# Performance work log

Measured on AMD Instinct MI355X. Metric: run time of the kernel, lower is better.

The kernel has to match this reference:

```python
import jax, jax.numpy as jnp
import numpy as np

BATCH = 2
SEQ = 2048
DIM = 2048
HEADS = 16
DIM_HEAD = 64
DIM_INNER = HEADS * DIM_HEAD  # 1024
SOFTCAP = 50.0
EPS = 1e-12


def setup_inputs() -> dict:
    key = jax.random.key(0)
    k1, k2, k3, k4 = jax.random.split(key, 4)
    x = jax.random.normal(k1, (BATCH, SEQ, DIM), dtype=jnp.float32)
    # RMSNorm gamma param (initialized near zero in the torch module)
    gamma = jax.random.normal(k2, (DIM,), dtype=jnp.float32) * 0.02
    # Linear weights stored already-transposed: x @ W
    w_qkv = jax.random.normal(k3, (DIM, 3 * DIM_INNER), dtype=jnp.float32) * (DIM ** -0.5)
    w_out = jax.random.normal(k4, (DIM_INNER, DIM), dtype=jnp.float32) * (DIM_INNER ** -0.5)
    # (type, offset, length) triples per batch; bidirectional attention inside each span
    modalities = jnp.array(
        [[[0, 256, 256], [0, 1024, 512]],
         [[0, 128, 256], [0, 1536, 384]]], dtype=jnp.int32)
    return dict(x=x, gamma=gamma, w_qkv=w_qkv, w_out=w_out, modalities=modalities)


def _transfusion_attn_mask(seq_len, modalities):
    # causal | (q in span AND kv in span)  -> Bool[b, i, j]
    seq = jnp.arange(seq_len)
    causal = seq[:, None] >= seq[None, :]                      # [i, j]
    offsets = modalities[..., 1]                                # [b, m]
    ends = offsets + modalities[..., 2]                         # [b, m]
    q_in = seq[None, None, :] >= offsets[..., None]             # [b, m, i]
    kv_in = seq[None, None, :] < ends[..., None]                # [b, m, j]
    is_modality = jnp.any(q_in[..., :, None] & kv_in[..., None, :], axis=1)  # [b, i, j]
    return causal[None] | is_modality


def _rmsnorm(x, gamma):
    n = jnp.sqrt(jnp.sum(x * x, axis=-1, keepdims=True))
    x = x / jnp.maximum(n, EPS)
    return x * (DIM ** 0.5) * (gamma + 1.0)


def reference(x, gamma, w_qkv, w_out, modalities):
    xn = _rmsnorm(x, gamma)
    qkv = xn @ w_qkv                                            # [b, n, 3*h*d]
    qkv = qkv.reshape(BATCH, SEQ, 3, HEADS, DIM_HEAD)
    qkv = jnp.transpose(qkv, (2, 0, 3, 1, 4))                   # [3, b, h, n, d]
    q, k, v = qkv[0], qkv[1], qkv[2]
    q = q * (DIM_HEAD ** -0.5)
    sim = jnp.einsum('bhid,bhjd->bhij', q, k)
    sim = jnp.tanh(sim / SOFTCAP) * SOFTCAP                     # softclamp
    mask = _transfusion_attn_mask(SEQ, modalities)              # [b, i, j]
    neg = -jnp.finfo(sim.dtype).max
    sim = jnp.where(mask[:, None, :, :], sim, neg)
    attn = jax.nn.softmax(sim, axis=-1)
    out = jnp.einsum('bhij,bhjd->bhid', attn, v)
    out = jnp.transpose(out, (0, 2, 1, 3)).reshape(BATCH, SEQ, DIM_INNER)
    return out @ w_out
```

## Files before the change

kernel.cpp:

```cpp
#include <hip/hip_runtime.h>
#include <hip/hip_bf16.h>

typedef unsigned short u16;
typedef unsigned int u32;
typedef __attribute__((ext_vector_type(8))) short short8;
typedef __attribute__((ext_vector_type(4))) float f32x4;
typedef __attribute__((ext_vector_type(4))) u16 u16x4;

#define DEV __device__ __forceinline__

DEV u16 f2bf(float f) {
    union { float f; u32 u; } v; v.f = f;
    u32 r = v.u;
    u32 lsb = (r >> 16) & 1u;
    r += 0x7fffu + lsb;
    return (u16)(r >> 16);
}

DEV void gload_lds16(const u16* g, u16* l) {
    __builtin_amdgcn_global_load_lds(
        (const __attribute__((address_space(1))) u32*)(const void*)g,
        (__attribute__((address_space(3))) u32*)(void*)l,
        16, 0, 0);
}

__global__ void prep(const float* __restrict__ x, const float* __restrict__ gamma,
                     const float* __restrict__ w_qkv, const float* __restrict__ w_out,
                     u16* __restrict__ xn, u16* __restrict__ wqkvT, u16* __restrict__ woutT) {
    __shared__ float tile[32][33];
    __shared__ float red[4];
    int id = blockIdx.x;
    int t = threadIdx.x;
    if (id < 8192) {
        const float* in; u16* out; int R, C, bx, by;
        if (id < 6144) { in = w_qkv; out = wqkvT; R = 2048; C = 3072; bx = id % 96; by = id / 96; }
        else { id -= 6144; in = w_out; out = woutT; R = 1024; C = 2048; bx = id % 64; by = id / 64; }
        int tx = t & 31, ty = t >> 5;
        int c0 = bx * 32, r0 = by * 32;
#pragma unroll
        for (int i = 0; i < 4; i++)
            tile[ty * 4 + i][tx] = in[(size_t)(r0 + ty * 4 + i) * C + c0 + tx];
        __syncthreads();
#pragma unroll
        for (int i = 0; i < 4; i++)
            out[(size_t)(c0 + ty * 4 + i) * R + r0 + tx] = f2bf(tile[tx][ty * 4 + i]);
    } else {
        int row = id - 8192;
        const float4* xr = (const float4*)(x + (size_t)row * 2048);
        float4 a = xr[t];
        float4 b = xr[256 + t];
        float ss = a.x * a.x + a.y * a.y + a.z * a.z + a.w * a.w +
                   b.x * b.x + b.y * b.y + b.z * b.z + b.w * b.w;
#pragma unroll
        for (int off = 32; off; off >>= 1) ss += __shfl_xor(ss, off);
        if ((t & 63) == 0) red[t >> 6] = ss;
        __syncthreads();
        float tot = red[0] + red[1] + red[2] + red[3];
        float n = sqrtf(tot);
        float inv = 45.254833995939045f / fmaxf(n, 1e-12f);
        const float4* gr = (const float4*)gamma;
        float4 g0 = gr[t], g1 = gr[256 + t];
        u16x4 o0 = { f2bf(a.x * inv * (g0.x + 1.f)), f2bf(a.y * inv * (g0.y + 1.f)),
                     f2bf(a.z * inv * (g0.z + 1.f)), f2bf(a.w * inv * (g0.w + 1.f)) };
        u16x4 o1 = { f2bf(b.x * inv * (g1.x + 1.f)), f2bf(b.y * inv * (g1.y + 1.f)),
                     f2bf(b.z * inv * (g1.z + 1.f)), f2bf(b.w * inv * (g1.w + 1.f)) };
        u16x4* xo = (u16x4*)(xn + (size_t)row * 2048);
        xo[t] = o0;
        xo[256 + t] = o1;
    }
}

template <int EPI, int BN, int CR, int CC>
__global__ __launch_bounds__(512, 6) void gemmw(
    const u16* __restrict__ A, const u16* __restrict__ BT,
    int M, int N, int K,
    float* __restrict__ Cout,
    u16* __restrict__ qb, u16* __restrict__ kb, u16* __restrict__ vT) {
    constexpr int NF = BN / 64;
    constexpr bool BX = (BN * 4) > 512;
    __shared__ __align__(16) u16 As[3][4096];
    __shared__ __align__(16) u16 Bs[3][BN * 32];
    int t = threadIdx.x, lane = t & 63, wid = t >> 6;
    int g = lane >> 4, r = lane & 15;
    int wm = wid >> 2, wn = wid & 3;
    int csw = (r >> 1) & 3;

    int id = blockIdx.x;
    int xcd = id & 7, slot = id >> 3;
    int by = (xcd >> 1) * CR + slot / CC;
    int bx = (xcd & 1) * CC + slot % CC;
    int brow = by * 128, bcol = bx * BN;

    int gk = (t & 3) ^ ((t >> 3) & 3);
    const u16* Ag = A + (size_t)(brow + (t >> 2)) * K + gk * 8;
    const u16* Bg = BT + (size_t)(bcol + (t >> 2)) * K + gk * 8;
    const u16* Bg2 = BT + (size_t)(bcol + 128 + (t >> 2)) * K + gk * 8;
    int dst = (t & ~63) * 8;

    f32x4 acc[4][NF] = {};
    short8 areg[4], breg[NF];
    int NT = K >> 5;

#define STG(kt_, b3_) { \
        gload_lds16(Ag + (kt_) * 32, &As[b3_][dst]); \
        gload_lds16(Bg + (kt_) * 32, &Bs[b3_][dst]); \
        if constexpr (BX) { if (t < 256) gload_lds16(Bg2 + (kt_) * 32, &Bs[b3_][4096 + dst]); } }
#define SCHEDB() __builtin_amdgcn_sched_barrier(0)
#define BAR() __builtin_amdgcn_s_barrier()

    STG(0, 0);
    if (NT > 1) STG(1, 1);
    asm volatile("s_waitcnt vmcnt(0)" ::: "memory");
    SCHEDB();
    BAR();

    int c0 = 0;
    for (int kt = 0; kt < NT; ++kt) {
        int c2 = c0 + 2; if (c2 >= 3) c2 -= 3;
        bool s1 = kt + 1 < NT, s2 = kt + 2 < NT;
        if (s2) STG(kt + 2, c2);
        const u16* Ac = As[c0];
        const u16* Bc = Bs[c0];
#pragma unroll
        for (int mf = 0; mf < 4; mf++)
            areg[mf] = *(const short8*)&Ac[(wm * 64 + mf * 16 + r) * 32 + (g ^ csw) * 8];
#pragma unroll
        for (int nf = 0; nf < NF; nf++)
            breg[nf] = *(const short8*)&Bc[(wn * (BN / 4) + nf * 16 + r) * 32 + (g ^ csw) * 8];
        asm volatile("s_waitcnt lgkmcnt(0)" ::: "memory");
        SCHEDB();
        __builtin_amdgcn_s_setprio(1);
#pragma unroll
        for (int mf = 0; mf < 4; mf++)
#pragma unroll
            for (int nf = 0; nf < NF; nf++)
                acc[mf][nf] = __builtin_amdgcn_mfma_f32_16x16x32_bf16(areg[mf], breg[nf], acc[mf][nf], 0, 0, 0);
        __builtin_amdgcn_s_setprio(0);
        if (s2) {
            if (BX && wid < 4) { asm volatile("s_waitcnt vmcnt(3)" ::: "memory"); }
            else               { asm volatile("s_waitcnt vmcnt(2)" ::: "memory"); }
        } else if (s1) {
            asm volatile("s_waitcnt vmcnt(0)" ::: "memory");
        }
        SCHEDB();
        BAR();
        c0 = (c0 + 1 == 3) ? 0 : c0 + 1;
    }
#undef STG
#undef SCHEDB
#undef BAR

    if (EPI == 0) {
#pragma unroll
        for (int mf = 0; mf < 4; mf++)
#pragma unroll
            for (int nf = 0; nf < NF; nf++) {
                int cb = bcol + wn * (BN / 4) + nf * 16 + r;
                int which = cb >> 10;
                int hd = cb & 1023;
                int hh = hd >> 6, d = hd & 63;
#pragma unroll
                for (int j = 0; j < 4; j++) {
                    int rr = brow + wm * 64 + mf * 16 + 4 * g + j;
                    int b = rr >> 11, nn = rr & 2047;
                    float v = acc[mf][nf][j];
                    size_t bh = (size_t)(b * 16 + hh);
                    if (which == 0)      qb[(bh * 2048 + nn) * 64 + d] = f2bf(v * 0.125f);
                    else if (which == 1) kb[(bh * 2048 + nn) * 64 + d] = f2bf(v);
                    else                 vT[(bh * 64 + d) * 2048 + nn] = f2bf(v);
                }
            }
    } else {
#pragma unroll
        for (int mf = 0; mf < 4; mf++)
#pragma unroll
            for (int nf = 0; nf < NF; nf++) {
                int cb = bcol + wn * (BN / 4) + nf * 16 + r;
#pragma unroll
                for (int j = 0; j < 4; j++) {
                    int rr = brow + wm * 64 + mf * 16 + 4 * g + j;
                    Cout[(size_t)rr * N + cb] = acc[mf][nf][j];
                }
            }
    }
}

__global__ __launch_bounds__(256, 3) void flash_attn(
    const u16* __restrict__ q, const u16* __restrict__ kk, const u16* __restrict__ vT,
    const int* __restrict__ mods, u16* __restrict__ attn_out) {
    __shared__ __align__(16) u16 Ks[2][4096];
    __shared__ __align__(16) u16 Vs[2][4096];
    __shared__ __align__(16) u16 Plds[4][2][16][72];
    int t = threadIdx.x, lane = t & 63, wave = t >> 6;
    int g = lane >> 4, r = lane & 15;
    int h = blockIdx.x, b = blockIdx.y;
    int qs = (15 - blockIdx.z) * 128;
    int bh = b * 16 + h;
    int qbase = qs + wave * 32;

    int off0 = mods[b * 6 + 1], end0 = off0 + mods[b * 6 + 2];
    int off1 = mods[b * 6 + 4], end1 = off1 + mods[b * 6 + 5];

    const u16* Qp = q + ((size_t)bh * 2048 + qbase) * 64;
    short8 qf0[2], qf1[2];
#pragma unroll
    for (int s = 0; s < 2; s++) {
        qf0[s] = *(const short8*)(Qp + (size_t)(s * 16 + r) * 64 + 8 * g);
        qf1[s] = *(const short8*)(Qp + (size_t)(s * 16 + r) * 64 + 32 + 8 * g);
    }

    int rowlim[2];
#pragma unroll
    for (int s = 0; s < 2; s++) {
        int iq = qbase + s * 16 + r;
        int lim0 = (iq >= off0) ? end0 : 0;
        int lim1 = (iq >= off1) ? end1 : 0;
        rowlim[s] = max(iq + 1, max(lim0, lim1));
    }

    int jlb = qs + 128;
    if (qs + 127 >= off0) jlb = max(jlb, end0);
    if (qs + 127 >= off1) jlb = max(jlb, end1);

    const u16* Kp = kk + (size_t)bh * 2048 * 64;
    const u16* Vp = vT + (size_t)bh * 64 * 2048;

    f32x4 ot[2][4] = {};
    float psA[2] = {}, psB[2] = {};
    int sw = r & 7;

    auto stage64 = [&](const u16* gbase, int gstride, u16* lds) {
#pragma unroll
        for (int i = 0; i < 2; i++) {
            int c = i * 256 + t;
            int row = c >> 3;
            int gsl = (c & 7) ^ (row & 7);
            gload_lds16(gbase + (size_t)row * gstride + 8 * gsl,
                        lds + (size_t)(c & ~63) * 8);
        }
    };

    stage64(Kp, 64, Ks[0]);
    stage64(Vp, 2048, Vs[0]);
    int buf = 0;

    for (int jb = 0; jb < jlb; jb += 64) {
        if (jb + 64 < jlb) {
            stage64(Kp + (size_t)(jb + 64) * 64, 64, Ks[buf ^ 1]);
            stage64(Vp + (jb + 64), 2048, Vs[buf ^ 1]);
            asm volatile("s_waitcnt vmcnt(4)" ::: "memory");
        } else {
            asm volatile("s_waitcnt vmcnt(0)" ::: "memory");
        }
        __builtin_amdgcn_s_barrier();
        const u16* Kt = Ks[buf];
        const u16* Vt = Vs[buf];

        f32x4 st[2][4];
#pragma unroll
        for (int tt = 0; tt < 4; tt++) {
            int row = 16 * tt + r;
            short8 kf0 = *(const short8*)&Kt[(size_t)(row * 8 + (g ^ sw)) * 8];
            short8 kf1 = *(const short8*)&Kt[(size_t)(row * 8 + ((4 + g) ^ sw)) * 8];
#pragma unroll
            for (int s = 0; s < 2; s++) {
                f32x4 z = {};
                z = __builtin_amdgcn_mfma_f32_16x16x32_bf16(kf0, qf0[s], z, 0, 0, 0);
                z = __builtin_amdgcn_mfma_f32_16x16x32_bf16(kf1, qf1[s], z, 0, 0, 0);
                st[s][tt] = z;
            }
        }
#pragma unroll
        for (int s = 0; s < 2; s++) {
            u16* Pws = &Plds[wave][s][0][0];
#pragma unroll
            for (int tt = 0; tt < 4; tt++) {
                int kvb = jb + 16 * tt + 4 * g;
                float p0, p1, p2, p3;
#pragma unroll
                for (int j = 0; j < 4; j++) {
                    float x = st[s][tt][j];
                    float x2 = x * x;
                    float inner = __builtin_fmaf(x2, 2.1333333e-8f, -1.3333333e-4f);
                    float poly = __builtin_fmaf(x2, inner, 1.0f);
                    float pv = __expf(x * poly);
                    pv = (kvb + j < rowlim[s]) ? pv : 0.f;
                    if (j == 0) p0 = pv; else if (j == 1) p1 = pv;
                    else if (j == 2) p2 = pv; else p3 = pv;
                }
                psA[s] += p0 + p1;
                psB[s] += p2 + p3;
                u32 pk0, pk1;
                asm("v_cvt_pk_bf16_f32 %0, %1, %2" : "=v"(pk0) : "v"(p0), "v"(p1));
                asm("v_cvt_pk_bf16_f32 %0, %1, %2" : "=v"(pk1) : "v"(p2), "v"(p3));
                *(u32*)&Pws[r * 72 + 16 * tt + 4 * g] = pk0;
                *(u32*)&Pws[r * 72 + 16 * tt + 4 * g + 2] = pk1;
            }
        }
        short8 pf0[2], pf1[2];
#pragma unroll
        for (int s = 0; s < 2; s++) {
            pf0[s] = *(const short8*)&Plds[wave][s][r][8 * g];
            pf1[s] = *(const short8*)&Plds[wave][s][r][32 + 8 * g];
        }
#pragma unroll
        for (int dt = 0; dt < 4; dt++) {
            int row = 16 * dt + r;
            short8 vf0 = *(const short8*)&Vt[(size_t)(row * 8 + (g ^ sw)) * 8];
            short8 vf1 = *(const short8*)&Vt[(size_t)(row * 8 + ((4 + g) ^ sw)) * 8];
#pragma unroll
            for (int s = 0; s < 2; s++) {
                ot[s][dt] = __builtin_amdgcn_mfma_f32_16x16x32_bf16(vf0, pf0[s], ot[s][dt], 0, 0, 0);
                ot[s][dt] = __builtin_amdgcn_mfma_f32_16x16x32_bf16(vf1, pf1[s], ot[s][dt], 0, 0, 0);
            }
        }
        asm volatile("s_waitcnt lgkmcnt(0)" ::: "memory");
        __builtin_amdgcn_s_barrier();
        buf ^= 1;
    }

#pragma unroll
    for (int s = 0; s < 2; s++) {
        float lrow = psA[s] + psB[s];
        lrow += __shfl_xor(lrow, 16);
        lrow += __shfl_xor(lrow, 32);
        float inv = 1.f / lrow;
        u16* Op = attn_out + ((size_t)(b * 2048 + qbase + s * 16 + r)) * 1024 + h * 64;
#pragma unroll
        for (int dt = 0; dt < 4; dt++) {
            u16x4 o = { f2bf(ot[s][dt][0] * inv), f2bf(ot[s][dt][1] * inv),
                        f2bf(ot[s][dt][2] * inv), f2bf(ot[s][dt][3] * inv) };
            *(u16x4*)(Op + dt * 16 + 4 * g) = o;
        }
    }
}

extern "C" void kernel_launch(void* const* d_in, const int* in_sizes, int n_in,
                              void* d_out, int out_size, void* d_ws, size_t ws_size,
                              hipStream_t stream) {
    const float* x = (const float*)d_in[0];
    const float* gamma = (const float*)d_in[1];
    const float* w_qkv = (const float*)d_in[2];
    const float* w_out = (const float*)d_in[3];
    const int* mods = (const int*)d_in[4];
    float* out = (float*)d_out;

    u16* ws = (u16*)d_ws;
    u16* xn    = ws;
    u16* wqkvT = ws + 8388608;
    u16* woutT = ws + 14680064;
    u16* qb    = ws + 16777216;
    u16* kb    = ws + 20971520;
    u16* vT    = ws + 25165824;
    u16* ao    = ws + 29360128;

    prep<<<dim3(12288), dim3(256), 0, stream>>>(x, gamma, w_qkv, w_out, xn, wqkvT, woutT);
    gemmw<0, 128, 8, 12><<<dim3(768), dim3(512), 0, stream>>>(xn, wqkvT, 4096, 3072, 2048,
                                                              nullptr, qb, kb, vT);
    flash_attn<<<dim3(16, 2, 16), dim3(256), 0, stream>>>(qb, kb, vT, mods, ao);
    gemmw<1, 128, 8, 8><<<dim3(512), dim3(512), 0, stream>>>(ao, woutT, 4096, 2048, 1024,
                                                             out, nullptr, nullptr, nullptr);
}
```

Before: 173.1 us.

## Load GEMM A operand directly from global into registers, bypassing LDS

The A tile is no longer staged through shared memory. Each wave now loads its own A fragments from global memory straight into registers, double-buffered two k-steps ahead, while B stays in the triple-buffered LDS pipeline. This removes the LDS writes and reads for A and shrinks shared memory use, which may allow more blocks per CU. In exchange it adds uncoalesced 16-byte global loads and extra register pressure. The BN>128 branch for loading B is dropped, and the loop is unrolled by two, which assumes NT is even.

```diff
diff --git a/kernel.cpp b/kernel.cpp
--- a/kernel.cpp
+++ b/kernel.cpp
@@ -77,8 +77,6 @@
     float* __restrict__ Cout,
     u16* __restrict__ qb, u16* __restrict__ kb, u16* __restrict__ vT) {
     constexpr int NF = BN / 64;
-    constexpr bool BX = (BN * 4) > 512;
-    __shared__ __align__(16) u16 As[3][4096];
     __shared__ __align__(16) u16 Bs[3][BN * 32];
     int t = threadIdx.x, lane = t & 63, wid = t >> 6;
     int g = lane >> 4, r = lane & 15;
@@ -92,63 +90,61 @@
     int brow = by * 128, bcol = bx * BN;
 
     int gk = (t & 3) ^ ((t >> 3) & 3);
-    const u16* Ag = A + (size_t)(brow + (t >> 2)) * K + gk * 8;
     const u16* Bg = BT + (size_t)(bcol + (t >> 2)) * K + gk * 8;
-    const u16* Bg2 = BT + (size_t)(bcol + 128 + (t >> 2)) * K + gk * 8;
     int dst = (t & ~63) * 8;
 
+    const u16* Arow0 = A + (size_t)(brow + wm * 64 + r) * K + g * 8;
+    const size_t r16K = (size_t)16 * K;
+
     f32x4 acc[4][NF] = {};
-    short8 areg[4], breg[NF];
+    short8 arA[4], arB[4], breg[NF];
     int NT = K >> 5;
 
-#define STG(kt_, b3_) { \
-        gload_lds16(Ag + (kt_) * 32, &As[b3_][dst]); \
-        gload_lds16(Bg + (kt_) * 32, &Bs[b3_][dst]); \
-        if constexpr (BX) { if (t < 256) gload_lds16(Bg2 + (kt_) * 32, &Bs[b3_][4096 + dst]); } }
+#define STGB(kt_, b3_) gload_lds16(Bg + (kt_) * 32, &Bs[b3_][dst]);
+#define LDA(dst_, kt_) { \
+    _Pragma("unroll") for (int mf = 0; mf < 4; mf++) \
+        dst_[mf] = *(const short8*)(Arow0 + (size_t)mf * r16K + (kt_) * 32); }
+#define MFMAS(ar_) { \
+    __builtin_amdgcn_s_setprio(1); \
+    _Pragma("unroll") for (int mf = 0; mf < 4; mf++) \
+    _Pragma("unroll") for (int nf = 0; nf < NF; nf++) \
+        acc[mf][nf] = __builtin_amdgcn_mfma_f32_16x16x32_bf16(ar_[mf], breg[nf], acc[mf][nf], 0, 0, 0); \
+    __builtin_amdgcn_s_setprio(0); }
 #define SCHEDB() __builtin_amdgcn_sched_barrier(0)
 #define BAR() __builtin_amdgcn_s_barrier()
-
-    STG(0, 0);
-    if (NT > 1) STG(1, 1);
-    asm volatile("s_waitcnt vmcnt(0)" ::: "memory");
+#define ITER(kt_, ar_) { \
+    int c2 = c0 + 2; if (c2 >= 3) c2 -= 3; \
+    bool s2 = (kt_) + 2 < NT; \
+    _Pragma("unroll") for (int nf = 0; nf < NF; nf++) \
+        breg[nf] = *(const short8*)&Bs[c0][(wn * (BN / 4) + nf * 16 + r) * 32 + (g ^ csw) * 8]; \
+    if (s2) STGB((kt_) + 2, c2); \
+    asm volatile("s_waitcnt lgkmcnt(0)" ::: "memory"); \
+    SCHEDB(); \
+    MFMAS(ar_); \
+    if (s2) { LDA(ar_, (kt_) + 2); asm volatile("s_waitcnt vmcnt(5)" ::: "memory"); } \
+    else    { asm volatile("s_waitcnt vmcnt(0)" ::: "memory"); } \
+    SCHEDB(); BAR(); \
+    c0 = (c0 + 1 == 3) ? 0 : c0 + 1; }
+
+    LDA(arA, 0);
+    STGB(0, 0);
+    if (NT > 1) { STGB(1, 1); LDA(arB, 1); }
+    if (NT > 1) { asm volatile("s_waitcnt vmcnt(5)" ::: "memory"); }
+    else        { asm volatile("s_waitcnt vmcnt(0)" ::: "memory"); }
     SCHEDB();
     BAR();
 
     int c0 = 0;
-    for (int kt = 0; kt < NT; ++kt) {
-        int c2 = c0 + 2; if (c2 >= 3) c2 -= 3;
-        bool s1 = kt + 1 < NT, s2 = kt + 2 < NT;
-        if (s2) STG(kt + 2, c2);
-        const u16* Ac = As[c0];
-        const u16* Bc = Bs[c0];
-#pragma unroll
-        for (int mf = 0; mf < 4; mf++)
-            areg[mf] = *(const short8*)&Ac[(wm * 64 + mf * 16 + r) * 32 + (g ^ csw) * 8];
-#pragma unroll
-        for (int nf = 0; nf < NF; nf++)
-            breg[nf] = *(const short8*)&Bc[(wn * (BN / 4) + nf * 16 + r) * 32 + (g ^ csw) * 8];
-        asm volatile("s_waitcnt lgkmcnt(0)" ::: "memory");
-        SCHEDB();
-        __builtin_amdgcn_s_setprio(1);
-#pragma unroll
-        for (int mf = 0; mf < 4; mf++)
-#pragma unroll
-            for (int nf = 0; nf < NF; nf++)
-                acc[mf][nf] = __builtin_amdgcn_mfma_f32_16x16x32_bf16(areg[mf], breg[nf], acc[mf][nf], 0, 0, 0);
-        __builtin_amdgcn_s_setprio(0);
-        if (s2) {
-            if (BX && wid < 4) { asm volatile("s_waitcnt vmcnt(3)" ::: "memory"); }
-            else               { asm volatile("s_waitcnt vmcnt(2)" ::: "memory"); }
-        } else if (s1) {
-            asm volatile("s_waitcnt vmcnt(0)" ::: "memory");
-        }
-        SCHEDB();
-        BAR();
-        c0 = (c0 + 1 == 3) ? 0 : c0 + 1;
-    }
-#undef STG
+    for (int kt = 0; kt < NT; kt += 2) {
+        ITER(kt, arA);
+        ITER(kt + 1, arB);
+    }
+#undef STGB
+#undef LDA
+#undef MFMAS
 #undef SCHEDB
 #undef BAR
+#undef ITER
 
     if (EPI == 0) {
 #pragma unroll
```

Result: slower. 481.4 us (+178.1%).
